# Kernel optimization log

Measured on AMD Instinct MI355X. Metric: run time of the kernel, lower is better.

The kernel has to match this reference:

```python
import jax, jax.numpy as jnp
import numpy as np

B, S, H = 4, 256, 8
N_MB, N_C = 50000, 1000
P, BS, CS, L0, L1, L2 = 32, 16, 16, 96, 32, 16


def setup_inputs() -> dict:
    key = jax.random.key(0)
    ks = jax.random.split(key, 12)
    sd = 0.02
    return {
        "attention_scores": jax.random.normal(ks[0], (B, H, S, S), dtype=jnp.float32),
        "b_seq": jax.random.randint(ks[1], (B, S), 0, N_MB + 1, dtype=jnp.int32),
        "c_seq": jax.random.randint(ks[2], (B, S), 0, N_C + 2, dtype=jnp.int32),
        "e_pos": jax.random.normal(ks[3], (S * 2, H, P), dtype=jnp.float32) * sd,
        "e_bi": jax.random.normal(ks[4], (N_MB + 1, H, BS), dtype=jnp.float32) * sd,
        "e_bj": jax.random.normal(ks[5], (N_MB + 1, H, BS), dtype=jnp.float32) * sd,
        "e_ci": jax.random.normal(ks[6], (N_C + 2, H, CS), dtype=jnp.float32) * sd,
        "e_cj": jax.random.normal(ks[7], (N_C + 2, H, CS), dtype=jnp.float32) * sd,
        "w1_e": jax.random.normal(ks[8], (L0, L1, H), dtype=jnp.float32) * sd,
        "w2_e": jax.random.normal(ks[9], (L1, L2, H), dtype=jnp.float32) * sd,
        "w3_e": jax.random.normal(ks[10], (L2, H), dtype=jnp.float32) * sd,
    }


def reference(attention_scores, b_seq, c_seq, e_pos, e_bi, e_bj, e_ci, e_cj, w1_e, w2_e, w3_e):
    b, h, s, _ = attention_scores.shape
    pos = jnp.arange(s, dtype=jnp.int32)
    # relative position index (i - j + seq_len), shared across batch: [S,S]
    f_pos = pos[:, None] - pos[None, :] + s
    emb_pos = e_pos[f_pos]                 # [S,S,H,P]
    emb_bi = e_bi[b_seq]                   # [B,S,H,BS]
    emb_bj = e_bj[b_seq]
    emb_ci = e_ci[c_seq]                   # [B,S,H,CS]
    emb_cj = e_cj[c_seq]
    # concat of broadcasted features -> e: [B,S,S,H,L0]
    e = jnp.concatenate([
        jnp.broadcast_to(emb_pos[None], (b, s, s, h, emb_pos.shape[-1])),
        jnp.broadcast_to(emb_bi[:, :, None], (b, s, s, h, emb_bi.shape[-1])),
        jnp.broadcast_to(emb_bj[:, None, :], (b, s, s, h, emb_bj.shape[-1])),
        jnp.broadcast_to(emb_ci[:, :, None], (b, s, s, h, emb_ci.shape[-1])),
        jnp.broadcast_to(emb_cj[:, None, :], (b, s, s, h, emb_cj.shape[-1])),
    ], axis=-1)
    e1 = jax.nn.relu(jnp.einsum('bmnhd,dkh->bmnhk', e, w1_e))
    e2 = jax.nn.relu(jnp.einsum('bmnhk,klh->bmnhl', e1, w2_e))
    da_score = jnp.einsum('bmnhk,kh->bhmn', e2, w3_e)
    return attention_scores + da_score
```

## Files before the change

### kernel.cpp

```cpp
#include <hip/hip_runtime.h>
#include <stdint.h>

typedef __attribute__((ext_vector_type(8))) short short8;
typedef __attribute__((ext_vector_type(4))) float f32x4;

#define SEQ 256
#define NH 8

__device__ __forceinline__ uint32_t cvt_pk_bf16(float lo, float hi) {
  uint32_t r;
  asm("v_cvt_pk_bf16_f32 %0, %1, %2" : "=v"(r) : "v"(lo), "v"(hi));
  return r;
}

__device__ __forceinline__ short8 pack8(f32x4 a, f32x4 b) {
  union { uint32_t u[4]; short8 v; } t;
  t.u[0] = cvt_pk_bf16(a[0], a[1]);
  t.u[1] = cvt_pk_bf16(a[2], a[3]);
  t.u[2] = cvt_pk_bf16(b[0], b[1]);
  t.u[3] = cvt_pk_bf16(b[2], b[3]);
  return t.v;
}

__global__ __launch_bounds__(512, 4) void dis_att_fused(
    const float* __restrict__ attn, const int* __restrict__ bseq,
    const int* __restrict__ cseq, const float* __restrict__ epos,
    const float* __restrict__ ebi, const float* __restrict__ ebj,
    const float* __restrict__ eci, const float* __restrict__ ecj,
    const float* __restrict__ w1, const float* __restrict__ w2,
    const float* __restrict__ w3, float* __restrict__ out) {
  __shared__ float sAp[128][36];
  __shared__ float sAi[64][36];
  __shared__ float sAj[64][36];
  int tid = threadIdx.x;
  int wg = blockIdx.x;
  int nt = wg & 3, mt = (wg >> 2) & 3, h = (wg >> 4) & 7, b = wg >> 7;
  int m0 = mt * 64, n0 = nt * 64;
  int f0 = m0 - n0 + 193;
  int lane = tid & 63, w = tid >> 6;
  int lcol = lane & 15, kb = lane >> 4, k8 = kb * 8;
  f32x4 zero = {0.f, 0.f, 0.f, 0.f};

  if (w < 4) {
    short8 bf[2];
#pragma unroll
    for (int kt = 0; kt < 2; ++kt) {
      union { uint32_t u[4]; short8 v; } t;
#pragma unroll
      for (int r = 0; r < 4; ++r) {
        float lo = w1[(k8 + 2 * r) * 256 + (kt * 16 + lcol) * 8 + h];
        float hi = w1[(k8 + 2 * r + 1) * 256 + (kt * 16 + lcol) * 8 + h];
        t.u[r] = cvt_pk_bf16(lo, hi);
      }
      bf[kt] = t.v;
    }
#pragma unroll
    for (int t = 0; t < 2; ++t) {
      int mt_ = w + t * 4;
      int frow = f0 + mt_ * 16 + lcol;
      if (frow > 511) frow = 511;
      const float* ep = epos + (frow * NH + h) * 32 + k8;
      short8 af = pack8(*(const f32x4*)ep, *(const f32x4*)(ep + 4));
#pragma unroll
      for (int kt = 0; kt < 2; ++kt) {
        f32x4 d = __builtin_amdgcn_mfma_f32_16x16x32_bf16(af, bf[kt], zero, 0, 0, 0);
#pragma unroll
        for (int r = 0; r < 4; ++r)
          sAp[mt_ * 16 + kb * 4 + r][kt * 16 + lcol] = d[r];
      }
    }
  } else {
    int isI = w < 6;
    int p0 = isI ? ((kb < 2 ? 32 : 48) + k8)
                 : ((kb < 2 ? 48 : 64) + k8);
    short8 bf[2];
#pragma unroll
    for (int kt = 0; kt < 2; ++kt) {
      union { uint32_t u[4]; short8 v; } t;
#pragma unroll
      for (int r = 0; r < 4; ++r) {
        float lo = w1[(p0 + 2 * r) * 256 + (kt * 16 + lcol) * 8 + h];
        float hi = w1[(p0 + 2 * r + 1) * 256 + (kt * 16 + lcol) * 8 + h];
        t.u[r] = cvt_pk_bf16(lo, hi);
      }
      bf[kt] = t.v;
    }
    const float* eB = isI ? ebi : ebj;
    const float* eC = isI ? eci : ecj;
    int base = isI ? m0 : n0;
    int w2_ = isI ? (w - 4) : (w - 6);
#pragma unroll
    for (int t = 0; t < 2; ++t) {
      int mt_ = w2_ * 2 + t;
      int gm = b * SEQ + base + mt_ * 16 + lcol;
      int bi = bseq[gm], ci = cseq[gm];
      const float* src = (kb < 2) ? eB + (bi * NH + h) * 16 + k8
                                  : eC + (ci * NH + h) * 16 + (k8 - 16);
      short8 af = pack8(*(const f32x4*)src, *(const f32x4*)(src + 4));
#pragma unroll
      for (int kt = 0; kt < 2; ++kt) {
        f32x4 d = __builtin_amdgcn_mfma_f32_16x16x32_bf16(af, bf[kt], zero, 0, 0, 0);
#pragma unroll
        for (int r = 0; r < 4; ++r) {
          float* T = isI ? &sAi[mt_ * 16 + kb * 4 + r][kt * 16 + lcol]
                         : &sAj[mt_ * 16 + kb * 4 + r][kt * 16 + lcol];
          *T = d[r];
        }
      }
    }
  }
  __syncthreads();

  union { uint32_t u[4]; short8 v; } w2f;
#pragma unroll
  for (int r = 0; r < 4; ++r) {
    float lo = w2[(k8 + 2 * r) * 128 + lcol * 8 + h];
    float hi = w2[(k8 + 2 * r + 1) * 128 + lcol * 8 + h];
    w2f.u[r] = cvt_pk_bf16(lo, hi);
  }
  float w3v[4];
#pragma unroll
  for (int r = 0; r < 4; ++r) w3v[r] = w3[(kb * 4 + r) * 8 + h];

  f32x4 ajA[4], ajB[4];
#pragma unroll
  for (int ng = 0; ng < 4; ++ng) {
    int nl = ng * 16 + lcol;
    ajA[ng] = *(const f32x4*)&sAj[nl][k8];
    ajB[ng] = *(const f32x4*)&sAj[nl][k8 + 4];
  }

  const float* attn_b = attn + (b * NH + h) * SEQ * SEQ;
  float* out_b = out + (b * NH + h) * SEQ * SEQ;
  int bit4 = kb & 1, bit5 = kb & 2;

#pragma unroll
  for (int s = 0; s < 2; ++s) {
    int mb = w * 8 + s * 4;
    float av[4];
    int idxs[4];
#pragma unroll
    for (int ng = 0; ng < 4; ++ng) {
      idxs[ng] = (m0 + mb + kb) * SEQ + n0 + ng * 16 + lcol;
      av[ng] = attn_b[idxs[ng]];
    }
    f32x4 aiA[4], aiB[4];
#pragma unroll
    for (int mi = 0; mi < 4; ++mi) {
      aiA[mi] = *(const f32x4*)&sAi[mb + mi][k8];
      aiB[mi] = *(const f32x4*)&sAi[mb + mi][k8 + 4];
    }
#pragma unroll
    for (int ng = 0; ng < 4; ++ng) {
      int nl = ng * 16 + lcol;
      f32x4 pA[4], pB[4];
#pragma unroll
      for (int mi = 0; mi < 4; ++mi) {
        int rl = mb + mi - nl + 63;
        pA[mi] = *(const f32x4*)&sAp[rl][k8];
        pB[mi] = *(const f32x4*)&sAp[rl][k8 + 4];
      }
      __builtin_amdgcn_sched_barrier(0);
      float part[4];
#pragma unroll
      for (int mi = 0; mi < 4; ++mi) {
        f32x4 s0 = pA[mi] + aiA[mi] + ajA[ng];
        f32x4 s1 = pB[mi] + aiB[mi] + ajB[ng];
        union { uint32_t u[4]; short8 v; } ef;
        ef.u[0] = cvt_pk_bf16(fmaxf(s0[0], 0.f), fmaxf(s0[1], 0.f));
        ef.u[1] = cvt_pk_bf16(fmaxf(s0[2], 0.f), fmaxf(s0[3], 0.f));
        ef.u[2] = cvt_pk_bf16(fmaxf(s1[0], 0.f), fmaxf(s1[1], 0.f));
        ef.u[3] = cvt_pk_bf16(fmaxf(s1[2], 0.f), fmaxf(s1[3], 0.f));
        f32x4 d = __builtin_amdgcn_mfma_f32_16x16x32_bf16(w2f.v, ef.v, zero, 0, 0, 0);
        part[mi] = fmaxf(d[0], 0.f) * w3v[0] + fmaxf(d[1], 0.f) * w3v[1] +
                   fmaxf(d[2], 0.f) * w3v[2] + fmaxf(d[3], 0.f) * w3v[3];
      }
      float mineA = bit4 ? part[1] : part[0];
      float sendA = bit4 ? part[0] : part[1];
      float mineB = bit4 ? part[3] : part[2];
      float sendB = bit4 ? part[2] : part[3];
      mineA += __shfl_xor(sendA, 16, 64);
      mineB += __shfl_xor(sendB, 16, 64);
      float keep = bit5 ? mineB : mineA;
      float send = bit5 ? mineA : mineB;
      float res = keep + __shfl_xor(send, 32, 64);
      out_b[idxs[ng]] = av[ng] + res;
    }
  }
}

extern "C" void kernel_launch(void* const* d_in, const int* in_sizes, int n_in,
                              void* d_out, int out_size, void* d_ws, size_t ws_size,
                              hipStream_t stream) {
  const float* attn = (const float*)d_in[0];
  const int* bseq   = (const int*)d_in[1];
  const int* cseq   = (const int*)d_in[2];
  const float* epos = (const float*)d_in[3];
  const float* ebi  = (const float*)d_in[4];
  const float* ebj  = (const float*)d_in[5];
  const float* eci  = (const float*)d_in[6];
  const float* ecj  = (const float*)d_in[7];
  const float* w1   = (const float*)d_in[8];
  const float* w2   = (const float*)d_in[9];
  const float* w3   = (const float*)d_in[10];
  float* out = (float*)d_out;

  hipLaunchKernelGGL(dis_att_fused, dim3(512), dim3(512), 0, stream,
                     attn, bseq, cseq, epos, ebi, ebj, eci, ecj, w1, w2, w3, out);
}
```

Before: 26.55 us.

## Precompute first-layer projection tables in a separate kernel before main fused pass

Moves the first-layer MFMA projections of the positional, b and c embeddings into a separate kernel that writes per-head tables to workspace. The main kernel then loads its tiles from those tables instead of recomputing them per workgroup. This removes the redundant projection work repeated across tiles (positional rows are recomputed per batch and tile), but adds a second launch and a global round trip for the tables.

Measured after the change: 25.66 us. 1.03x faster.

```diff
diff --git a/kernel.cpp b/kernel.cpp
--- a/kernel.cpp
+++ b/kernel.cpp
@@ -22,14 +22,82 @@
   return t.v;
 }
 
-__global__ __launch_bounds__(512, 4) void dis_att_fused(
-    const float* __restrict__ attn, const int* __restrict__ bseq,
-    const int* __restrict__ cseq, const float* __restrict__ epos,
-    const float* __restrict__ ebi, const float* __restrict__ ebj,
-    const float* __restrict__ eci, const float* __restrict__ ecj,
-    const float* __restrict__ w1, const float* __restrict__ w2,
-    const float* __restrict__ w3, float* __restrict__ out) {
-  __shared__ float sAp[128][36];
+__global__ __launch_bounds__(256) void build_tables_mfma(
+    const int* __restrict__ bseq, const int* __restrict__ cseq,
+    const float* __restrict__ epos, const float* __restrict__ ebi,
+    const float* __restrict__ ebj, const float* __restrict__ eci,
+    const float* __restrict__ ecj, const float* __restrict__ w1,
+    float* __restrict__ Tpos, float* __restrict__ Ti, float* __restrict__ Tj) {
+  int lane = threadIdx.x & 63, w = threadIdx.x >> 6;
+  int task = blockIdx.x * 4 + w;
+  int lcol = lane & 15, kb = lane >> 4, k8 = kb * 8;
+  f32x4 zero = {0.f, 0.f, 0.f, 0.f};
+
+  if (task < 256) {
+    int h = task >> 5, ft = task & 31;
+    short8 bf[2];
+#pragma unroll
+    for (int kt = 0; kt < 2; ++kt) {
+      union { uint32_t u[4]; short8 v; } t;
+#pragma unroll
+      for (int r = 0; r < 4; ++r) {
+        float lo = w1[(k8 + 2 * r) * 256 + (kt * 16 + lcol) * 8 + h];
+        float hi = w1[(k8 + 2 * r + 1) * 256 + (kt * 16 + lcol) * 8 + h];
+        t.u[r] = cvt_pk_bf16(lo, hi);
+      }
+      bf[kt] = t.v;
+    }
+    const float* ep = epos + ((ft * 16 + lcol) * NH + h) * 32 + k8;
+    short8 af = pack8(*(const f32x4*)ep, *(const f32x4*)(ep + 4));
+#pragma unroll
+    for (int kt = 0; kt < 2; ++kt) {
+      f32x4 d = __builtin_amdgcn_mfma_f32_16x16x32_bf16(af, bf[kt], zero, 0, 0, 0);
+#pragma unroll
+      for (int r = 0; r < 4; ++r)
+        Tpos[h * 16384 + (ft * 16 + kb * 4 + r) * 32 + kt * 16 + lcol] = d[r];
+    }
+  } else {
+    int isI = task < 768;
+    int t2 = task - (isI ? 256 : 768);
+    int h = t2 >> 6, bm = t2 & 63;
+    int p0 = isI ? ((kb < 2 ? 32 : 48) + k8)
+                 : ((kb < 2 ? 48 : 64) + k8);
+    short8 bf[2];
+#pragma unroll
+    for (int kt = 0; kt < 2; ++kt) {
+      union { uint32_t u[4]; short8 v; } t;
+#pragma unroll
+      for (int r = 0; r < 4; ++r) {
+        float lo = w1[(p0 + 2 * r) * 256 + (kt * 16 + lcol) * 8 + h];
+        float hi = w1[(p0 + 2 * r + 1) * 256 + (kt * 16 + lcol) * 8 + h];
+        t.u[r] = cvt_pk_bf16(lo, hi);
+      }
+      bf[kt] = t.v;
+    }
+    int gm = bm * 16 + lcol;
+    int bi = bseq[gm], ci = cseq[gm];
+    const float* eB = isI ? ebi : ebj;
+    const float* eC = isI ? eci : ecj;
+    const float* src = (kb < 2) ? eB + (bi * NH + h) * 16 + k8
+                                : eC + (ci * NH + h) * 16 + (k8 - 16);
+    short8 af = pack8(*(const f32x4*)src, *(const f32x4*)(src + 4));
+    float* T = isI ? Ti : Tj;
+#pragma unroll
+    for (int kt = 0; kt < 2; ++kt) {
+      f32x4 d = __builtin_amdgcn_mfma_f32_16x16x32_bf16(af, bf[kt], zero, 0, 0, 0);
+#pragma unroll
+      for (int r = 0; r < 4; ++r)
+        T[h * 32768 + (bm * 16 + kb * 4 + r) * 32 + kt * 16 + lcol] = d[r];
+    }
+  }
+}
+
+__global__ __launch_bounds__(512, 4) void dis_att_main(
+    const float* __restrict__ attn, const float* __restrict__ w2,
+    const float* __restrict__ w3, const float* __restrict__ Tpos,
+    const float* __restrict__ Ti, const float* __restrict__ Tj,
+    float* __restrict__ out) {
+  __shared__ float sAp[127][36];
   __shared__ float sAi[64][36];
   __shared__ float sAj[64][36];
   int tid = threadIdx.x;
@@ -37,79 +105,23 @@
   int nt = wg & 3, mt = (wg >> 2) & 3, h = (wg >> 4) & 7, b = wg >> 7;
   int m0 = mt * 64, n0 = nt * 64;
   int f0 = m0 - n0 + 193;
+
+  {
+    int r = tid >> 3, q = tid & 7;
+    const float* P = Tpos + h * 16384 + (f0 + r) * 32 + q * 4;
+    *(f32x4*)&sAp[r][q * 4] = *(const f32x4*)P;
+    if (r + 64 < 127)
+      *(f32x4*)&sAp[r + 64][q * 4] = *(const f32x4*)(P + 64 * 32);
+    *(f32x4*)&sAi[r][q * 4] =
+        *(const f32x4*)(Ti + h * 32768 + (b * 256 + m0 + r) * 32 + q * 4);
+    *(f32x4*)&sAj[r][q * 4] =
+        *(const f32x4*)(Tj + h * 32768 + (b * 256 + n0 + r) * 32 + q * 4);
+  }
+  __syncthreads();
+
   int lane = tid & 63, w = tid >> 6;
   int lcol = lane & 15, kb = lane >> 4, k8 = kb * 8;
   f32x4 zero = {0.f, 0.f, 0.f, 0.f};
-
-  if (w < 4) {
-    short8 bf[2];
-#pragma unroll
-    for (int kt = 0; kt < 2; ++kt) {
-      union { uint32_t u[4]; short8 v; } t;
-#pragma unroll
-      for (int r = 0; r < 4; ++r) {
-        float lo = w1[(k8 + 2 * r) * 256 + (kt * 16 + lcol) * 8 + h];
-        float hi = w1[(k8 + 2 * r + 1) * 256 + (kt * 16 + lcol) * 8 + h];
-        t.u[r] = cvt_pk_bf16(lo, hi);
-      }
-      bf[kt] = t.v;
-    }
-#pragma unroll
-    for (int t = 0; t < 2; ++t) {
-      int mt_ = w + t * 4;
-      int frow = f0 + mt_ * 16 + lcol;
-      if (frow > 511) frow = 511;
-      const float* ep = epos + (frow * NH + h) * 32 + k8;
-      short8 af = pack8(*(const f32x4*)ep, *(const f32x4*)(ep + 4));
-#pragma unroll
-      for (int kt = 0; kt < 2; ++kt) {
-        f32x4 d = __builtin_amdgcn_mfma_f32_16x16x32_bf16(af, bf[kt], zero, 0, 0, 0);
-#pragma unroll
-        for (int r = 0; r < 4; ++r)
-          sAp[mt_ * 16 + kb * 4 + r][kt * 16 + lcol] = d[r];
-      }
-    }
-  } else {
-    int isI = w < 6;
-    int p0 = isI ? ((kb < 2 ? 32 : 48) + k8)
-                 : ((kb < 2 ? 48 : 64) + k8);
-    short8 bf[2];
-#pragma unroll
-    for (int kt = 0; kt < 2; ++kt) {
-      union { uint32_t u[4]; short8 v; } t;
-#pragma unroll
-      for (int r = 0; r < 4; ++r) {
-        float lo = w1[(p0 + 2 * r) * 256 + (kt * 16 + lcol) * 8 + h];
-        float hi = w1[(p0 + 2 * r + 1) * 256 + (kt * 16 + lcol) * 8 + h];
-        t.u[r] = cvt_pk_bf16(lo, hi);
-      }
-      bf[kt] = t.v;
-    }
-    const float* eB = isI ? ebi : ebj;
-    const float* eC = isI ? eci : ecj;
-    int base = isI ? m0 : n0;
-    int w2_ = isI ? (w - 4) : (w - 6);
-#pragma unroll
-    for (int t = 0; t < 2; ++t) {
-      int mt_ = w2_ * 2 + t;
-      int gm = b * SEQ + base + mt_ * 16 + lcol;
-      int bi = bseq[gm], ci = cseq[gm];
-      const float* src = (kb < 2) ? eB + (bi * NH + h) * 16 + k8
-                                  : eC + (ci * NH + h) * 16 + (k8 - 16);
-      short8 af = pack8(*(const f32x4*)src, *(const f32x4*)(src + 4));
-#pragma unroll
-      for (int kt = 0; kt < 2; ++kt) {
-        f32x4 d = __builtin_amdgcn_mfma_f32_16x16x32_bf16(af, bf[kt], zero, 0, 0, 0);
-#pragma unroll
-        for (int r = 0; r < 4; ++r) {
-          float* T = isI ? &sAi[mt_ * 16 + kb * 4 + r][kt * 16 + lcol]
-                         : &sAj[mt_ * 16 + kb * 4 + r][kt * 16 + lcol];
-          *T = d[r];
-        }
-      }
-    }
-  }
-  __syncthreads();
 
   union { uint32_t u[4]; short8 v; } w2f;
 #pragma unroll
@@ -205,6 +217,12 @@
   const float* w3   = (const float*)d_in[10];
   float* out = (float*)d_out;
 
-  hipLaunchKernelGGL(dis_att_fused, dim3(512), dim3(512), 0, stream,
-                     attn, bseq, cseq, epos, ebi, ebj, eci, ecj, w1, w2, w3, out);
-}
+  float* Tpos = (float*)d_ws;
+  float* Ti   = Tpos + 131072;
+  float* Tj   = Ti + 262144;
+
+  hipLaunchKernelGGL(build_tables_mfma, dim3(320), dim3(256), 0, stream,
+                     bseq, cseq, epos, ebi, ebj, eci, ecj, w1, Tpos, Ti, Tj);
+  hipLaunchKernelGGL(dis_att_main, dim3(512), dim3(512), 0, stream,
+                     attn, w2, w3, Tpos, Ti, Tj, out);
+}
```
